# Kernel optimization log

Measured on AMD Instinct MI355X. Metric: run time of the kernel, lower is better.

Reference implementation:

```python
import jax, jax.numpy as jnp
import numpy as np

B, C, Wd, Hd = 128, 2048, 14, 14
S, L, M = 312, 300, 1024  # attributes, w2v length, med_dim
RATIO = 1.0               # attritube_num != 85 branch


def setup_inputs() -> dict:
    key = jax.random.key(0)
    ks = jax.random.split(key, 12)
    return {
        "feat": jax.random.normal(ks[0], (B, C, Wd, Hd), dtype=jnp.float32),
        "w2v_att": jax.random.normal(ks[1], (S, L), dtype=jnp.float32),
        "Wq": jax.random.normal(ks[2], (L, M), dtype=jnp.float32) * (1.0 / np.sqrt(L)),
        "bq": jax.random.normal(ks[3], (M,), dtype=jnp.float32) * 0.01,
        "Wk": jax.random.normal(ks[4], (C, M), dtype=jnp.float32) * (1.0 / np.sqrt(C)),
        "bk": jax.random.normal(ks[5], (M,), dtype=jnp.float32) * 0.01,
        "Wv": jax.random.normal(ks[6], (C, M), dtype=jnp.float32) * (1.0 / np.sqrt(C)),
        "bv": jax.random.normal(ks[7], (M,), dtype=jnp.float32) * 0.01,
        "Wo": jax.random.normal(ks[8], (M, C), dtype=jnp.float32) * (1.0 / np.sqrt(M)),
        "bo": jax.random.normal(ks[9], (C,), dtype=jnp.float32) * 0.01,
        "V_att_final": jax.random.normal(ks[10], (S, C), dtype=jnp.float32),
    }


def reference(feat, w2v_att, Wq, bq, Wk, bk, Wv, bv, Wo, bo, V_att_final):
    # feat: [B, C, W, H] -> [B, C, N]
    b, c = feat.shape[0], feat.shape[1]
    f = feat.reshape(b, c, -1)
    # Q from attribute word vectors: [S, M]
    query = w2v_att @ Wq + bq
    # K, V from spatial features: [B, N, M]
    key = jnp.einsum('bcn,cm->bnm', f, Wk) + bk
    value = jnp.einsum('bcn,cm->bnm', f, Wv) + bv
    # attention over spatial locations: [B, S, N]
    scores = jnp.einsum('sm,bnm->bsn', query, key)
    attention = jax.nn.softmax(scores, axis=-1)
    # attended features -> output projection: [B, S, C]
    attented = jnp.einsum('bsn,bnm->bsm', attention, value)
    attented_o = jnp.einsum('bsm,mc->bsc', attented, Wo) + bo
    # global average pool over spatial dims: [B, C]
    feat_pool = jnp.mean(f, axis=2)
    final = feat_pool[:, None, :] + RATIO * attented_o  # [B, S, C]
    # einsum classifier (hid_dim == 0 branch): [B, S]
    v2s = jnp.einsum('bsc,sc->bs', final, V_att_final)
    return v2s
```

## Files before the change

kernel.cpp:

```cpp
#include <hip/hip_runtime.h>
#include <hip/hip_bf16.h>

namespace {
constexpr int Bn = 128, Cn = 2048, Nn = 196, Sn = 312, Ln = 300, Mn = 1024;
constexpr int Sp = 320, Lp = 320, PR = 192;

constexpr size_t OFF_F16   = 0;
constexpr size_t OFF_POOLX = OFF_F16   + (size_t)Bn*Nn*Cn/2;
constexpr size_t OFF_HC    = OFF_POOLX + (size_t)PR*Cn/2;
constexpr size_t OFF_WVM   = OFF_HC    + (size_t)Cn*Lp/2;
constexpr size_t OFF_V16   = OFF_WVM   + (size_t)Sp*Mn/2;
constexpr size_t OFF_WV16  = OFF_V16   + (size_t)Sp*Cn/2;
constexpr size_t OFF_W2V   = OFF_WV16  + (size_t)Cn*Mn/2;
constexpr size_t OFF_BQK   = OFF_W2V   + (size_t)Sp*Lp/2;
constexpr size_t OFF_QK    = OFF_BQK   + Cn;
constexpr size_t OFF_WWT   = OFF_QK    + (size_t)Sp*Cn/2;
constexpr size_t OFF_PVF   = OFF_WWT   + (size_t)Sp*Cn/2;
}

typedef __attribute__((ext_vector_type(8))) short u16x8;
typedef __attribute__((ext_vector_type(8))) _Float16 f16x8;
typedef __attribute__((ext_vector_type(4))) _Float16 f16x4;
typedef __attribute__((ext_vector_type(4))) float f32x4;

__device__ __forceinline__ f16x8 as_h(u16x8 v) { return __builtin_bit_cast(f16x8, v); }

__device__ __forceinline__ void gload16(void* lds, const void* g) {
    __builtin_amdgcn_global_load_lds(
        (const __attribute__((address_space(1))) void*)g,
        (__attribute__((address_space(3))) void*)lds, 16, 0, 0);
}

__device__ __forceinline__ void stage_rows(ushort* lds, const ushort* src,
                                           size_t row0, int k0, int ld,
                                           int tid, int nslots) {
    int base = 0;
    for (; base + 256 <= nslots; base += 256) {
        const int slot = base + tid;
        const int r = slot >> 2, q = (slot & 3) ^ ((r >> 1) & 3);
        gload16(lds + (size_t)(base + (tid & 192)) * 8,
                src + (row0 + r) * (size_t)ld + k0 + q * 8);
    }
    const int rem = nslots - base;
    if (rem && tid < rem) {
        const int slot = base + tid;
        const int r = slot >> 2, q = (slot & 3) ^ ((r >> 1) & 3);
        gload16(lds + (size_t)base * 8,
                src + (row0 + r) * (size_t)ld + k0 + q * 8);
    }
}

__device__ __forceinline__ u16x8 frag_ld(const ushort* tile, int fr, int lane) {
    const int rl = lane & 15;
    const int q  = (lane >> 4) ^ ((rl >> 1) & 3);
    return *(const u16x8*)(tile + ((fr * 16 + rl) * 32 + q * 8));
}

__device__ __forceinline__ void mini16(
        const ushort* __restrict__ A, int lda, const ushort* __restrict__ B, int ldb,
        int r0, int c0, int K, const float* __restrict__ bias,
        _Float16* __restrict__ outh, float* __restrict__ outf, int ldo,
        ushort* sA, ushort* sB, int tid) {
    const int lane = tid & 63, wid = tid >> 6;
    f32x4 acc[2][2];
    #pragma unroll
    for (int i = 0; i < 2; ++i)
        #pragma unroll
        for (int j = 0; j < 2; ++j) acc[i][j] = (f32x4)0.f;
    const int fa = (wid >> 1) * 2, fb = (wid & 1) * 2;
    for (int k0 = 0; k0 < K; k0 += 32) {
        stage_rows(sA, A, r0, k0, lda, tid, 256);
        stage_rows(sB, B, c0, k0, ldb, tid, 256);
        __syncthreads();
        f16x8 a0 = as_h(frag_ld(sA, fa, lane)), a1 = as_h(frag_ld(sA, fa + 1, lane));
        f16x8 b0 = as_h(frag_ld(sB, fb, lane)), b1 = as_h(frag_ld(sB, fb + 1, lane));
        acc[0][0] = __builtin_amdgcn_mfma_f32_16x16x32_f16(a0, b0, acc[0][0], 0, 0, 0);
        acc[0][1] = __builtin_amdgcn_mfma_f32_16x16x32_f16(a0, b1, acc[0][1], 0, 0, 0);
        acc[1][0] = __builtin_amdgcn_mfma_f32_16x16x32_f16(a1, b0, acc[1][0], 0, 0, 0);
        acc[1][1] = __builtin_amdgcn_mfma_f32_16x16x32_f16(a1, b1, acc[1][1], 0, 0, 0);
        __syncthreads();
    }
    #pragma unroll
    for (int i = 0; i < 2; ++i)
        #pragma unroll
        for (int j = 0; j < 2; ++j)
            #pragma unroll
            for (int rr = 0; rr < 4; ++rr) {
                const size_t row = r0 + (wid >> 1) * 32 + i * 16 + (lane >> 4) * 4 + rr;
                const int col = c0 + (wid & 1) * 32 + j * 16 + (lane & 15);
                const float v = acc[i][j][rr] + (bias ? bias[col] : 0.f);
                if (outh) outh[row * ldo + col] = (_Float16)v;
                else      outf[row * ldo + col] = v;
            }
}

__device__ __forceinline__ void mini_f32in(
        const float* __restrict__ A, int lda, int RA,
        const float* __restrict__ B, int ldb, int RB,
        int r0, int c0, int K, _Float16* __restrict__ out, int ldo,
        ushort* sA, ushort* sB, int tid) {
    const int lane = tid & 63, wid = tid >> 6;
    f32x4 acc[2][2];
    #pragma unroll
    for (int i = 0; i < 2; ++i)
        #pragma unroll
        for (int j = 0; j < 2; ++j) acc[i][j] = (f32x4)0.f;
    const int fa = (wid >> 1) * 2, fb = (wid & 1) * 2;
    for (int k0 = 0; k0 < K; k0 += 32) {
        #pragma unroll
        for (int p = 0; p < 2; ++p) {
            const int e = tid + p * 256;
            const int r = e >> 3, k4 = (e & 7) * 4;
            const int ad = r * 32 + (((k4 >> 3) ^ ((r >> 1) & 3)) << 3) + (k4 & 7);
            float4 va = (r0 + r < RA) ? *(const float4*)&A[(size_t)(r0 + r) * lda + k0 + k4]
                                      : make_float4(0.f, 0.f, 0.f, 0.f);
            f16x4 ha;
            ha[0] = (_Float16)va.x; ha[1] = (_Float16)va.y;
            ha[2] = (_Float16)va.z; ha[3] = (_Float16)va.w;
            *(f16x4*)&sA[ad] = ha;
            float4 vb = (c0 + r < RB) ? *(const float4*)&B[(size_t)(c0 + r) * ldb + k0 + k4]
                                      : make_float4(0.f, 0.f, 0.f, 0.f);
            f16x4 hb;
            hb[0] = (_Float16)vb.x; hb[1] = (_Float16)vb.y;
            hb[2] = (_Float16)vb.z; hb[3] = (_Float16)vb.w;
            *(f16x4*)&sB[ad] = hb;
        }
        __syncthreads();
        f16x8 a0 = as_h(frag_ld(sA, fa, lane)), a1 = as_h(frag_ld(sA, fa + 1, lane));
        f16x8 b0 = as_h(frag_ld(sB, fb, lane)), b1 = as_h(frag_ld(sB, fb + 1, lane));
        acc[0][0] = __builtin_amdgcn_mfma_f32_16x16x32_f16(a0, b0, acc[0][0], 0, 0, 0);
        acc[0][1] = __builtin_amdgcn_mfma_f32_16x16x32_f16(a0, b1, acc[0][1], 0, 0, 0);
        acc[1][0] = __builtin_amdgcn_mfma_f32_16x16x32_f16(a1, b0, acc[1][0], 0, 0, 0);
        acc[1][1] = __builtin_amdgcn_mfma_f32_16x16x32_f16(a1, b1, acc[1][1], 0, 0, 0);
        __syncthreads();
    }
    #pragma unroll
    for (int i = 0; i < 2; ++i)
        #pragma unroll
        for (int j = 0; j < 2; ++j)
            #pragma unroll
            for (int rr = 0; rr < 4; ++rr) {
                const size_t row = r0 + (wid >> 1) * 32 + i * 16 + (lane >> 4) * 4 + rr;
                const int col = c0 + (wid & 1) * 32 + j * 16 + (lane & 15);
                out[row * ldo + col] = (_Float16)acc[i][j][rr];
            }
}

__global__ __launch_bounds__(256) void k_stageA(
        const float* __restrict__ feat, const float* __restrict__ w2v,
        const float* __restrict__ Wq,  const float* __restrict__ bq,
        const float* __restrict__ Wk,  const float* __restrict__ Wv,
        const float* __restrict__ bv,  const float* __restrict__ Wo,
        const float* __restrict__ bo,  const float* __restrict__ Vf,
        _Float16* __restrict__ f16, _Float16* __restrict__ poolx,
        _Float16* __restrict__ hc, _Float16* __restrict__ wvm,
        _Float16* __restrict__ v16, _Float16* __restrict__ wv16,
        _Float16* __restrict__ w2v16, float* __restrict__ bqk) {
    __shared__ __align__(16) char smem[51456];
    const int tid = threadIdx.x;
    int i = blockIdx.x;
    if (i < 8) {
        const int c = i * 256 + tid;
        float acc = bo[c];
        #pragma unroll 8
        for (int m = 0; m < Mn; ++m) acc = fmaf(bv[m], Wo[(size_t)m * Cn + c], acc);
        poolx[(size_t)128 * Cn + c] = (_Float16)acc;
    } else if ((i -= 8) < 512) {
        const int lane = tid & 63;
        const int c = i * 4 + (tid >> 6);
        float acc = 0.f;
        for (int m = lane; m < Mn; m += 64) acc = fmaf(bq[m], Wk[(size_t)c * Mn + m], acc);
        #pragma unroll
        for (int mm = 32; mm; mm >>= 1) acc += __shfl_xor(acc, mm);
        if (lane == 0) bqk[c] = acc;
    } else if ((i -= 512) < 160) {
        ushort* sA = (ushort*)smem;
        mini_f32in(Wk, Mn, 1 << 30, Wq, Mn, Ln,
                   (i / 5) * 64, (i % 5) * 64, Mn, hc, Lp, sA, sA + 2048, tid);
    } else if ((i -= 160) < 80) {
        ushort* sA = (ushort*)smem;
        mini_f32in(Vf, Cn, Sn, Wo, Cn, 1 << 30,
                   (i / 16) * 64, (i % 16) * 64, Cn, wvm, Mn, sA, sA + 2048, tid);
    } else if ((i -= 80) < 640) {
        const size_t idx = ((size_t)i * 256 + tid) * 4;
        const int r = (int)(idx >> 11);
        float4 v = (r < Sn) ? *(const float4*)&Vf[idx] : make_float4(0.f, 0.f, 0.f, 0.f);
        f16x4 h;
        h[0] = (_Float16)v.x; h[1] = (_Float16)v.y; h[2] = (_Float16)v.z; h[3] = (_Float16)v.w;
        *(f16x4*)&v16[idx] = h;
    } else if ((i -= 640) < 2048) {
        const size_t idx = ((size_t)i * 256 + tid) * 4;
        const float4 v = *(const float4*)&Wv[idx];
        f16x4 h;
        h[0] = (_Float16)v.x; h[1] = (_Float16)v.y; h[2] = (_Float16)v.z; h[3] = (_Float16)v.w;
        *(f16x4*)&wv16[idx] = h;
    } else if ((i -= 2048) < 100) {
        const int e0 = (i * 256 + tid) * 4;
        #pragma unroll
        for (int k = 0; k < 4; ++k) {
            const int e = e0 + k;
            const int r = e / Lp, cl = e - r * Lp;
            w2v16[e] = (r < Sn && cl < Ln) ? (_Float16)w2v[(size_t)r * Ln + cl] : (_Float16)0.f;
        }
    } else {
        i -= 100;
        float (*t)[197] = (float(*)[197])smem;
        float (*pp)[4]  = (float(*)[4])(smem + 64 * 197 * 4);
        const int b = i >> 5, c0 = (i & 31) * 64;
        for (int idx = tid; idx < 64 * 49; idx += 256) {
            const int r = idx / 49, nq = idx - r * 49;
            const float4 v = *(const float4*)&feat[((size_t)b * Cn + c0 + r) * Nn + nq * 4];
            t[r][nq * 4 + 0] = v.x; t[r][nq * 4 + 1] = v.y;
            t[r][nq * 4 + 2] = v.z; t[r][nq * 4 + 3] = v.w;
        }
        __syncthreads();
        {
            const int c = tid >> 2, q = tid & 3;
            float s = 0.f;
            #pragma unroll
            for (int n = 0; n < 49; ++n) s += t[c][q * 49 + n];
            pp[c][q] = s;
        }
        for (int idx = tid; idx < Nn * 32; idx += 256) {
            const int n = idx >> 5, cp = (idx & 31) * 2;
            f16x4 h;
            h[0] = (_Float16)t[cp][n]; h[1] = (_Float16)t[cp + 1][n];
            *(uint*)&f16[((size_t)b * Nn + n) * Cn + c0 + cp] = *(uint*)&h;
        }
        __syncthreads();
        if (tid < 64)
            poolx[(size_t)b * Cn + c0 + tid] =
                (_Float16)((pp[tid][0] + pp[tid][1] + pp[tid][2] + pp[tid][3]) * (1.0f / Nn));
    }
}

__global__ __launch_bounds__(256) void k_stageB(
        const ushort* __restrict__ w2v16, const ushort* __restrict__ hc,
        const float* __restrict__ bqk, const ushort* __restrict__ wvm,
        const ushort* __restrict__ wv16, const ushort* __restrict__ poolx,
        const ushort* __restrict__ v16,
        _Float16* __restrict__ qk16, _Float16* __restrict__ wwt16,
        float* __restrict__ pvf) {
    __shared__ __align__(16) ushort sA[2048], sB[2048];
    const int tid = threadIdx.x;
    int i = blockIdx.x;
    if (i < 160) {
        mini16(w2v16, Lp, hc, Lp, (i / 32) * 64, (i % 32) * 64, Lp,
               bqk, qk16, nullptr, Cn, sA, sB, tid);
    } else if ((i -= 160) < 160) {
        mini16(wvm, Mn, wv16, Mn, (i / 32) * 64, (i % 32) * 64, Mn,
               nullptr, wwt16, nullptr, Cn, sA, sB, tid);
    } else {
        i -= 160;
        mini16(poolx, Cn, v16, Cn, (i / 5) * 64, (i % 5) * 64, Cn,
               nullptr, nullptr, pvf, Sp, sA, sB, tid);
    }
}

__global__ __launch_bounds__(256) void k_attn(
        const _Float16* __restrict__ f16, const _Float16* __restrict__ qk16,
        const _Float16* __restrict__ ww16, const float* __restrict__ pvf,
        float* __restrict__ out) {
    __shared__ __align__(16) ushort smem[2][10752];
    const int tid = threadIdx.x, lane = tid & 63, wid = tid >> 6;
    const int id = blockIdx.x;
    const int xcd = id & 7, slot = id >> 3;
    const int b  = xcd * 16 + slot / 5;
    const int s0 = (slot % 5) * 64;
    const size_t frow0 = (size_t)b * Nn;

    f32x4 sc[13], vw[13];
    #pragma unroll
    for (int j = 0; j < 13; ++j) { sc[j] = (f32x4)0.f; vw[j] = (f32x4)0.f; }

    auto stage3 = [&](int p, int k0) {
        ushort* s = smem[p];
        stage_rows(s,        (const ushort*)f16,  frow0, k0, Cn, tid, 832);
        stage_rows(s + 6656, (const ushort*)qk16, s0,    k0, Cn, tid, 256);
        stage_rows(s + 8704, (const ushort*)ww16, s0,    k0, Cn, tid, 256);
    };

    constexpr int NIT = Cn / 32;
    stage3(0, 0);
    for (int t = 0; t < NIT; ++t) {
        const int cur = t & 1;
        __syncthreads();
        if (t + 1 < NIT) stage3(cur ^ 1, (t + 1) * 32);
        const ushort* sF = smem[cur];
        const f16x8 qf = as_h(frag_ld(sF + 6656, wid, lane));
        const f16x8 wf = as_h(frag_ld(sF + 8704, wid, lane));
        #pragma unroll
        for (int j = 0; j < 13; ++j) {
            const f16x8 ff = as_h(frag_ld(sF, j, lane));
            sc[j] = __builtin_amdgcn_mfma_f32_16x16x32_f16(qf, ff, sc[j], 0, 0, 0);
            vw[j] = __builtin_amdgcn_mfma_f32_16x16x32_f16(wf, ff, vw[j], 0, 0, 0);
        }
    }

    const int g = lane & 15;
    #pragma unroll
    for (int rr = 0; rr < 4; ++rr) {
        float mx = -1e30f;
        #pragma unroll
        for (int j = 0; j < 13; ++j)
            if (j < 12 || g < 4) mx = fmaxf(mx, sc[j][rr]);
        #pragma unroll
        for (int mm = 1; mm < 16; mm <<= 1) mx = fmaxf(mx, __shfl_xor(mx, mm));
        float den = 0.f, num = 0.f;
        #pragma unroll
        for (int j = 0; j < 13; ++j)
            if (j < 12 || g < 4) {
                const float e = __expf(sc[j][rr] - mx);
                den += e;
                num = fmaf(e, vw[j][rr], num);
            }
        #pragma unroll
        for (int mm = 1; mm < 16; mm <<= 1) {
            den += __shfl_xor(den, mm);
            num += __shfl_xor(num, mm);
        }
        if (g == 0) {
            const int s = s0 + wid * 16 + (lane >> 4) * 4 + rr;
            if (s < Sn)
                out[(size_t)b * Sn + s] =
                    pvf[(size_t)b * Sp + s] + pvf[(size_t)128 * Sp + s] + num / den;
        }
    }
}

extern "C" void kernel_launch(void* const* d_in, const int* in_sizes, int n_in,
                              void* d_out, int out_size, void* d_ws, size_t ws_size,
                              hipStream_t stream) {
    (void)in_sizes; (void)n_in; (void)ws_size; (void)out_size;
    const float* feat = (const float*)d_in[0];
    const float* w2v  = (const float*)d_in[1];
    const float* Wq   = (const float*)d_in[2];
    const float* bq   = (const float*)d_in[3];
    const float* Wk   = (const float*)d_in[4];
    const float* Wv   = (const float*)d_in[6];
    const float* bv   = (const float*)d_in[7];
    const float* Wo   = (const float*)d_in[8];
    const float* bo   = (const float*)d_in[9];
    const float* Vf   = (const float*)d_in[10];
    float* out = (float*)d_out;
    float* ws  = (float*)d_ws;

    _Float16* f16   = (_Float16*)(ws + OFF_F16);
    _Float16* poolx = (_Float16*)(ws + OFF_POOLX);
    _Float16* hc    = (_Float16*)(ws + OFF_HC);
    _Float16* wvm   = (_Float16*)(ws + OFF_WVM);
    _Float16* v16   = (_Float16*)(ws + OFF_V16);
    _Float16* wv16  = (_Float16*)(ws + OFF_WV16);
    _Float16* w2v16 = (_Float16*)(ws + OFF_W2V);
    float*    bqk   = ws + OFF_BQK;
    _Float16* qk16  = (_Float16*)(ws + OFF_QK);
    _Float16* wwt16 = (_Float16*)(ws + OFF_WWT);
    float*    pvf   = ws + OFF_PVF;

    k_stageA<<<dim3(8 + 512 + 160 + 80 + 640 + 2048 + 100 + 4096), 256, 0, stream>>>(
        feat, w2v, Wq, bq, Wk, Wv, bv, Wo, bo, Vf,
        f16, poolx, hc, wvm, v16, wv16, w2v16, bqk);
    k_stageB<<<dim3(160 + 160 + 15), 256, 0, stream>>>(
        (const ushort*)w2v16, (const ushort*)hc, bqk, (const ushort*)wvm,
        (const ushort*)wv16, (const ushort*)poolx, (const ushort*)v16,
        qk16, wwt16, pvf);
    k_attn<<<dim3(640), 256, 0, stream>>>(f16, qk16, wwt16, pvf, out);
}
```

Before: 247.8 us.

## Fuse fp16 feature conversion and pooled term into attention kernel

Drops the separate pass that transposed and converted feat to an fp16 [B,N,C] buffer and computed pooled features. The attention kernel now reads fp32 feat directly, converts and transposes it into LDS through a register-staged double buffer, and computes the pooled·V term with an extra MFMA over the same feature tiles. The bias constant (bo·V plus bv·Wo·V) is computed per attribute in a small reduction. This removes a large intermediate write and read of the features, at the cost of more register pressure, larger LDS use and extra conversion work inside the main loop.

Result: slower. 271.7 us (+9.6%).

```diff
diff --git a/kernel.cpp b/kernel.cpp
--- a/kernel.cpp
+++ b/kernel.cpp
@@ -3,24 +3,23 @@
 
 namespace {
 constexpr int Bn = 128, Cn = 2048, Nn = 196, Sn = 312, Ln = 300, Mn = 1024;
-constexpr int Sp = 320, Lp = 320, PR = 192;
-
-constexpr size_t OFF_F16   = 0;
-constexpr size_t OFF_POOLX = OFF_F16   + (size_t)Bn*Nn*Cn/2;
-constexpr size_t OFF_HC    = OFF_POOLX + (size_t)PR*Cn/2;
-constexpr size_t OFF_WVM   = OFF_HC    + (size_t)Cn*Lp/2;
-constexpr size_t OFF_V16   = OFF_WVM   + (size_t)Sp*Mn/2;
-constexpr size_t OFF_WV16  = OFF_V16   + (size_t)Sp*Cn/2;
-constexpr size_t OFF_W2V   = OFF_WV16  + (size_t)Cn*Mn/2;
-constexpr size_t OFF_BQK   = OFF_W2V   + (size_t)Sp*Lp/2;
-constexpr size_t OFF_QK    = OFF_BQK   + Cn;
-constexpr size_t OFF_WWT   = OFF_QK    + (size_t)Sp*Cn/2;
-constexpr size_t OFF_PVF   = OFF_WWT   + (size_t)Sp*Cn/2;
+constexpr int Sp = 320, Lp = 320;
+
+constexpr size_t OFF_HC   = 0;
+constexpr size_t OFF_WVM  = OFF_HC  + (size_t)Cn*Lp/2;
+constexpr size_t OFF_V16  = OFF_WVM + (size_t)Sp*Mn/2;
+constexpr size_t OFF_WV16 = OFF_V16 + (size_t)Sp*Cn/2;
+constexpr size_t OFF_W2V  = OFF_WV16+ (size_t)Cn*Mn/2;
+constexpr size_t OFF_BQK  = OFF_W2V + (size_t)Sp*Lp/2;
+constexpr size_t OFF_QK   = OFF_BQK + Cn;
+constexpr size_t OFF_WWT  = OFF_QK  + (size_t)Sp*Cn/2;
+constexpr size_t OFF_CST  = OFF_WWT + (size_t)Sp*Cn/2;
 }
 
 typedef __attribute__((ext_vector_type(8))) short u16x8;
 typedef __attribute__((ext_vector_type(8))) _Float16 f16x8;
 typedef __attribute__((ext_vector_type(4))) _Float16 f16x4;
+typedef __attribute__((ext_vector_type(2))) _Float16 f16x2;
 typedef __attribute__((ext_vector_type(4))) float f32x4;
 
 __device__ __forceinline__ f16x8 as_h(u16x8 v) { return __builtin_bit_cast(f16x8, v); }
@@ -147,25 +146,23 @@
 }
 
 __global__ __launch_bounds__(256) void k_stageA(
-        const float* __restrict__ feat, const float* __restrict__ w2v,
-        const float* __restrict__ Wq,  const float* __restrict__ bq,
-        const float* __restrict__ Wk,  const float* __restrict__ Wv,
-        const float* __restrict__ bv,  const float* __restrict__ Wo,
-        const float* __restrict__ bo,  const float* __restrict__ Vf,
-        _Float16* __restrict__ f16, _Float16* __restrict__ poolx,
+        const float* __restrict__ w2v, const float* __restrict__ Wq,
+        const float* __restrict__ bq,  const float* __restrict__ Wk,
+        const float* __restrict__ Wv,  const float* __restrict__ Wo,
+        const float* __restrict__ Vf,
         _Float16* __restrict__ hc, _Float16* __restrict__ wvm,
         _Float16* __restrict__ v16, _Float16* __restrict__ wv16,
         _Float16* __restrict__ w2v16, float* __restrict__ bqk) {
-    __shared__ __align__(16) char smem[51456];
+    __shared__ __align__(16) ushort sm[4096];
     const int tid = threadIdx.x;
     int i = blockIdx.x;
-    if (i < 8) {
-        const int c = i * 256 + tid;
-        float acc = bo[c];
-        #pragma unroll 8
-        for (int m = 0; m < Mn; ++m) acc = fmaf(bv[m], Wo[(size_t)m * Cn + c], acc);
-        poolx[(size_t)128 * Cn + c] = (_Float16)acc;
-    } else if ((i -= 8) < 512) {
+    if (i < 160) {
+        mini_f32in(Wk, Mn, 1 << 30, Wq, Mn, Ln,
+                   (i / 5) * 64, (i % 5) * 64, Mn, hc, Lp, sm, sm + 2048, tid);
+    } else if ((i -= 160) < 80) {
+        mini_f32in(Vf, Cn, Sn, Wo, Cn, 1 << 30,
+                   (i / 16) * 64, (i % 16) * 64, Cn, wvm, Mn, sm, sm + 2048, tid);
+    } else if ((i -= 80) < 512) {
         const int lane = tid & 63;
         const int c = i * 4 + (tid >> 6);
         float acc = 0.f;
@@ -173,15 +170,7 @@
         #pragma unroll
         for (int mm = 32; mm; mm >>= 1) acc += __shfl_xor(acc, mm);
         if (lane == 0) bqk[c] = acc;
-    } else if ((i -= 512) < 160) {
-        ushort* sA = (ushort*)smem;
-        mini_f32in(Wk, Mn, 1 << 30, Wq, Mn, Ln,
-                   (i / 5) * 64, (i % 5) * 64, Mn, hc, Lp, sA, sA + 2048, tid);
-    } else if ((i -= 160) < 80) {
-        ushort* sA = (ushort*)smem;
-        mini_f32in(Vf, Cn, Sn, Wo, Cn, 1 << 30,
-                   (i / 16) * 64, (i % 16) * 64, Cn, wvm, Mn, sA, sA + 2048, tid);
-    } else if ((i -= 80) < 640) {
+    } else if ((i -= 512) < 640) {
         const size_t idx = ((size_t)i * 256 + tid) * 4;
         const int r = (int)(idx >> 11);
         float4 v = (r < Sn) ? *(const float4*)&Vf[idx] : make_float4(0.f, 0.f, 0.f, 0.f);
@@ -194,7 +183,8 @@
         f16x4 h;
         h[0] = (_Float16)v.x; h[1] = (_Float16)v.y; h[2] = (_Float16)v.z; h[3] = (_Float16)v.w;
         *(f16x4*)&wv16[idx] = h;
-    } else if ((i -= 2048) < 100) {
+    } else {
+        i -= 2048;
         const int e0 = (i * 256 + tid) * 4;
         #pragma unroll
         for (int k = 0; k < 4; ++k) {
@@ -202,99 +192,124 @@
             const int r = e / Lp, cl = e - r * Lp;
             w2v16[e] = (r < Sn && cl < Ln) ? (_Float16)w2v[(size_t)r * Ln + cl] : (_Float16)0.f;
         }
-    } else {
-        i -= 100;
-        float (*t)[197] = (float(*)[197])smem;
-        float (*pp)[4]  = (float(*)[4])(smem + 64 * 197 * 4);
-        const int b = i >> 5, c0 = (i & 31) * 64;
-        for (int idx = tid; idx < 64 * 49; idx += 256) {
-            const int r = idx / 49, nq = idx - r * 49;
-            const float4 v = *(const float4*)&feat[((size_t)b * Cn + c0 + r) * Nn + nq * 4];
-            t[r][nq * 4 + 0] = v.x; t[r][nq * 4 + 1] = v.y;
-            t[r][nq * 4 + 2] = v.z; t[r][nq * 4 + 3] = v.w;
-        }
-        __syncthreads();
-        {
-            const int c = tid >> 2, q = tid & 3;
-            float s = 0.f;
-            #pragma unroll
-            for (int n = 0; n < 49; ++n) s += t[c][q * 49 + n];
-            pp[c][q] = s;
-        }
-        for (int idx = tid; idx < Nn * 32; idx += 256) {
-            const int n = idx >> 5, cp = (idx & 31) * 2;
-            f16x4 h;
-            h[0] = (_Float16)t[cp][n]; h[1] = (_Float16)t[cp + 1][n];
-            *(uint*)&f16[((size_t)b * Nn + n) * Cn + c0 + cp] = *(uint*)&h;
-        }
-        __syncthreads();
-        if (tid < 64)
-            poolx[(size_t)b * Cn + c0 + tid] =
-                (_Float16)((pp[tid][0] + pp[tid][1] + pp[tid][2] + pp[tid][3]) * (1.0f / Nn));
     }
 }
 
 __global__ __launch_bounds__(256) void k_stageB(
         const ushort* __restrict__ w2v16, const ushort* __restrict__ hc,
         const float* __restrict__ bqk, const ushort* __restrict__ wvm,
-        const ushort* __restrict__ wv16, const ushort* __restrict__ poolx,
-        const ushort* __restrict__ v16,
+        const ushort* __restrict__ wv16,
+        const float* __restrict__ bo, const float* __restrict__ Vf,
+        const float* __restrict__ bv,
         _Float16* __restrict__ qk16, _Float16* __restrict__ wwt16,
-        float* __restrict__ pvf) {
+        float* __restrict__ cst) {
     __shared__ __align__(16) ushort sA[2048], sB[2048];
     const int tid = threadIdx.x;
     int i = blockIdx.x;
     if (i < 160) {
+        mini16(wvm, Mn, wv16, Mn, (i / 32) * 64, (i % 32) * 64, Mn,
+               nullptr, wwt16, nullptr, Cn, sA, sB, tid);
+    } else if ((i -= 160) < 160) {
         mini16(w2v16, Lp, hc, Lp, (i / 32) * 64, (i % 32) * 64, Lp,
                bqk, qk16, nullptr, Cn, sA, sB, tid);
-    } else if ((i -= 160) < 160) {
-        mini16(wvm, Mn, wv16, Mn, (i / 32) * 64, (i % 32) * 64, Mn,
-               nullptr, wwt16, nullptr, Cn, sA, sB, tid);
     } else {
         i -= 160;
-        mini16(poolx, Cn, v16, Cn, (i / 5) * 64, (i % 5) * 64, Cn,
-               nullptr, nullptr, pvf, Sp, sA, sB, tid);
+        const int lane = tid & 63, wid = tid >> 6;
+        const int s = i * 4 + wid;
+        if (s >= Sn) return;
+        float part = 0.f;
+        for (int c = lane; c < Cn; c += 64) part = fmaf(bo[c], Vf[(size_t)s * Cn + c], part);
+        for (int m = lane; m < Mn; m += 64)
+            part = fmaf(bv[m], (float)*(const _Float16*)&wvm[(size_t)s * Mn + m], part);
+        #pragma unroll
+        for (int mm = 32; mm; mm >>= 1) part += __shfl_xor(part, mm);
+        if (lane == 0) cst[s] = part;
     }
 }
 
 __global__ __launch_bounds__(256) void k_attn(
-        const _Float16* __restrict__ f16, const _Float16* __restrict__ qk16,
-        const _Float16* __restrict__ ww16, const float* __restrict__ pvf,
-        float* __restrict__ out) {
-    __shared__ __align__(16) ushort smem[2][10752];
+        const float* __restrict__ feat, const _Float16* __restrict__ qk16,
+        const _Float16* __restrict__ ww16, const _Float16* __restrict__ v16,
+        const float* __restrict__ cst, float* __restrict__ out) {
+    __shared__ __align__(16) ushort smem[2][12800];
     const int tid = threadIdx.x, lane = tid & 63, wid = tid >> 6;
     const int id = blockIdx.x;
     const int xcd = id & 7, slot = id >> 3;
     const int b  = xcd * 16 + slot / 5;
     const int s0 = (slot % 5) * 64;
-    const size_t frow0 = (size_t)b * Nn;
-
-    f32x4 sc[13], vw[13];
+    const float* featb = feat + (size_t)b * Cn * Nn;
+
+    for (int u = tid; u < 384; u += 256) {
+        const int bf = u / 192, w = u - bf * 192;
+        *(uint*)&smem[bf][196 * 32 + w * 2] = 0u;
+    }
+
+    f32x4 sc[13], vw[13], gv = (f32x4)0.f;
     #pragma unroll
     for (int j = 0; j < 13; ++j) { sc[j] = (f32x4)0.f; vw[j] = (f32x4)0.f; }
 
-    auto stage3 = [&](int p, int k0) {
-        ushort* s = smem[p];
-        stage_rows(s,        (const ushort*)f16,  frow0, k0, Cn, tid, 832);
-        stage_rows(s + 6656, (const ushort*)qk16, s0,    k0, Cn, tid, 256);
-        stage_rows(s + 8704, (const ushort*)ww16, s0,    k0, Cn, tid, 256);
+    const int p = tid & 15, grp = tid >> 4;
+    float4 lo[4], hi[4];
+
+    auto loadF = [&](int k0) {
+        #pragma unroll
+        for (int it = 0; it < 4; ++it) {
+            const int qp = grp + 16 * it;
+            if (qp < 49) {
+                lo[it] = *(const float4*)&featb[(size_t)(k0 + 2 * p) * Nn + qp * 4];
+                hi[it] = *(const float4*)&featb[(size_t)(k0 + 2 * p + 1) * Nn + qp * 4];
+            }
+        }
     };
+    auto writeF = [&](int pb) {
+        ushort* s = smem[pb];
+        #pragma unroll
+        for (int it = 0; it < 4; ++it) {
+            const int qp = grp + 16 * it;
+            if (qp < 49) {
+                const float* fl = (const float*)&lo[it];
+                const float* fh = (const float*)&hi[it];
+                #pragma unroll
+                for (int k = 0; k < 4; ++k) {
+                    const int r = qp * 4 + k;
+                    const int qs = (p >> 2) ^ ((r >> 1) & 3);
+                    f16x2 h; h[0] = (_Float16)fl[k]; h[1] = (_Float16)fh[k];
+                    *(uint*)&s[r * 32 + qs * 8 + 2 * (p & 3)] = __builtin_bit_cast(uint, h);
+                }
+            }
+        }
+    };
+    auto stageQWV = [&](int pb, int k0) {
+        ushort* s = smem[pb];
+        stage_rows(s + 6656,  (const ushort*)qk16, s0, k0, Cn, tid, 256);
+        stage_rows(s + 8704,  (const ushort*)ww16, s0, k0, Cn, tid, 256);
+        stage_rows(s + 10752, (const ushort*)v16,  s0, k0, Cn, tid, 256);
+    };
+
+    loadF(0);
+    writeF(0);
+    stageQWV(0, 0);
 
     constexpr int NIT = Cn / 32;
-    stage3(0, 0);
     for (int t = 0; t < NIT; ++t) {
         const int cur = t & 1;
         __syncthreads();
-        if (t + 1 < NIT) stage3(cur ^ 1, (t + 1) * 32);
+        if (t + 1 < NIT) {
+            loadF((t + 1) * 32);
+            stageQWV(cur ^ 1, (t + 1) * 32);
+        }
         const ushort* sF = smem[cur];
-        const f16x8 qf = as_h(frag_ld(sF + 6656, wid, lane));
-        const f16x8 wf = as_h(frag_ld(sF + 8704, wid, lane));
+        const f16x8 qf = as_h(frag_ld(sF + 6656,  wid, lane));
+        const f16x8 wf = as_h(frag_ld(sF + 8704,  wid, lane));
+        const f16x8 vf = as_h(frag_ld(sF + 10752, wid, lane));
         #pragma unroll
         for (int j = 0; j < 13; ++j) {
             const f16x8 ff = as_h(frag_ld(sF, j, lane));
             sc[j] = __builtin_amdgcn_mfma_f32_16x16x32_f16(qf, ff, sc[j], 0, 0, 0);
             vw[j] = __builtin_amdgcn_mfma_f32_16x16x32_f16(wf, ff, vw[j], 0, 0, 0);
-        }
+            gv    = __builtin_amdgcn_mfma_f32_16x16x32_f16(vf, ff, gv,    0, 0, 0);
+        }
+        if (t + 1 < NIT) writeF(cur ^ 1);
     }
 
     const int g = lane & 15;
@@ -314,16 +329,17 @@
                 den += e;
                 num = fmaf(e, vw[j][rr], num);
             }
+        float gs = gv[rr];
         #pragma unroll
         for (int mm = 1; mm < 16; mm <<= 1) {
             den += __shfl_xor(den, mm);
             num += __shfl_xor(num, mm);
+            gs  += __shfl_xor(gs, mm);
         }
         if (g == 0) {
             const int s = s0 + wid * 16 + (lane >> 4) * 4 + rr;
             if (s < Sn)
-                out[(size_t)b * Sn + s] =
-                    pvf[(size_t)b * Sp + s] + pvf[(size_t)128 * Sp + s] + num / den;
+                out[(size_t)b * Sn + s] = cst[s] + gs * (1.0f / Nn) + num / den;
         }
     }
 }
@@ -345,8 +361,6 @@
     float* out = (float*)d_out;
     float* ws  = (float*)d_ws;
 
-    _Float16* f16   = (_Float16*)(ws + OFF_F16);
-    _Float16* poolx = (_Float16*)(ws + OFF_POOLX);
     _Float16* hc    = (_Float16*)(ws + OFF_HC);
     _Float16* wvm   = (_Float16*)(ws + OFF_WVM);
     _Float16* v16   = (_Float16*)(ws + OFF_V16);
@@ -355,14 +369,12 @@
     float*    bqk   = ws + OFF_BQK;
     _Float16* qk16  = (_Float16*)(ws + OFF_QK);
     _Float16* wwt16 = (_Float16*)(ws + OFF_WWT);
-    float*    pvf   = ws + OFF_PVF;
-
-    k_stageA<<<dim3(8 + 512 + 160 + 80 + 640 + 2048 + 100 + 4096), 256, 0, stream>>>(
-        feat, w2v, Wq, bq, Wk, Wv, bv, Wo, bo, Vf,
-        f16, poolx, hc, wvm, v16, wv16, w2v16, bqk);
-    k_stageB<<<dim3(160 + 160 + 15), 256, 0, stream>>>(
+    float*    cst   = ws + OFF_CST;
+
+    k_stageA<<<dim3(160 + 80 + 512 + 640 + 2048 + 100), 256, 0, stream>>>(
+        w2v, Wq, bq, Wk, Wv, Wo, Vf, hc, wvm, v16, wv16, w2v16, bqk);
+    k_stageB<<<dim3(160 + 160 + 78), 256, 0, stream>>>(
         (const ushort*)w2v16, (const ushort*)hc, bqk, (const ushort*)wvm,
-        (const ushort*)wv16, (const ushort*)poolx, (const ushort*)v16,
-        qk16, wwt16, pvf);
-    k_attn<<<dim3(640), 256, 0, stream>>>(f16, qk16, wwt16, pvf, out);
-}
+        (const ushort*)wv16, bo, Vf, bv, qk16, wwt16, cst);
+    k_attn<<<dim3(640), 256, 0, stream>>>(feat, qk16, wwt16, v16, cst, out);
+}
```

## Tile f16 feature layout into 64-channel blocks and double-buffer stage GEMMs

Applied to the files above, without the earlier changes.

The transposed fp16 feature buffer is stored as contiguous 196x64 channel blocks per batch, so k_attn loads each K-slice from a compact region instead of striding across full 2048-channel rows. The mini16 GEMM gains LDS double buffering with one barrier per iteration, and mini_f32in prefetches the next fp32 tile into registers before the MFMAs. Stage-B blocks are reordered so the long K=2048 pooled-feature GEMM launches first. This adds LDS and register pressure, and the new addressing must stay consistent between the producer and consumer of the feature buffer.

Result: faster. 216.6 us (median of 2 runs) (-12.6%).

```diff
diff --git a/kernel.cpp b/kernel.cpp
--- a/kernel.cpp
+++ b/kernel.cpp
@@ -60,7 +60,7 @@
         const ushort* __restrict__ A, int lda, const ushort* __restrict__ B, int ldb,
         int r0, int c0, int K, const float* __restrict__ bias,
         _Float16* __restrict__ outh, float* __restrict__ outf, int ldo,
-        ushort* sA, ushort* sB, int tid) {
+        ushort* sm, int tid) {
     const int lane = tid & 63, wid = tid >> 6;
     f32x4 acc[2][2];
     #pragma unroll
@@ -68,17 +68,24 @@
         #pragma unroll
         for (int j = 0; j < 2; ++j) acc[i][j] = (f32x4)0.f;
     const int fa = (wid >> 1) * 2, fb = (wid & 1) * 2;
-    for (int k0 = 0; k0 < K; k0 += 32) {
-        stage_rows(sA, A, r0, k0, lda, tid, 256);
-        stage_rows(sB, B, c0, k0, ldb, tid, 256);
-        __syncthreads();
+    const int NI = K / 32;
+    stage_rows(sm,        A, r0, 0, lda, tid, 256);
+    stage_rows(sm + 2048, B, c0, 0, ldb, tid, 256);
+    for (int t = 0; t < NI; ++t) {
+        const int cur = (t & 1) * 4096;
+        __syncthreads();
+        if (t + 1 < NI) {
+            stage_rows(sm + (cur ^ 4096),        A, r0, (t + 1) * 32, lda, tid, 256);
+            stage_rows(sm + (cur ^ 4096) + 2048, B, c0, (t + 1) * 32, ldb, tid, 256);
+        }
+        const ushort* sA = sm + cur;
+        const ushort* sB = sm + cur + 2048;
         f16x8 a0 = as_h(frag_ld(sA, fa, lane)), a1 = as_h(frag_ld(sA, fa + 1, lane));
         f16x8 b0 = as_h(frag_ld(sB, fb, lane)), b1 = as_h(frag_ld(sB, fb + 1, lane));
         acc[0][0] = __builtin_amdgcn_mfma_f32_16x16x32_f16(a0, b0, acc[0][0], 0, 0, 0);
         acc[0][1] = __builtin_amdgcn_mfma_f32_16x16x32_f16(a0, b1, acc[0][1], 0, 0, 0);
         acc[1][0] = __builtin_amdgcn_mfma_f32_16x16x32_f16(a1, b0, acc[1][0], 0, 0, 0);
         acc[1][1] = __builtin_amdgcn_mfma_f32_16x16x32_f16(a1, b1, acc[1][1], 0, 0, 0);
-        __syncthreads();
     }
     #pragma unroll
     for (int i = 0; i < 2; ++i)
@@ -106,26 +113,37 @@
         #pragma unroll
         for (int j = 0; j < 2; ++j) acc[i][j] = (f32x4)0.f;
     const int fa = (wid >> 1) * 2, fb = (wid & 1) * 2;
+
+    float4 va[2], vb[2];
+    auto loadregs = [&](int k0) {
+        #pragma unroll
+        for (int p = 0; p < 2; ++p) {
+            const int e = tid + p * 256;
+            const int r = e >> 3, k4 = (e & 7) * 4;
+            va[p] = (r0 + r < RA) ? *(const float4*)&A[(size_t)(r0 + r) * lda + k0 + k4]
+                                  : make_float4(0.f, 0.f, 0.f, 0.f);
+            vb[p] = (c0 + r < RB) ? *(const float4*)&B[(size_t)(c0 + r) * ldb + k0 + k4]
+                                  : make_float4(0.f, 0.f, 0.f, 0.f);
+        }
+    };
+    loadregs(0);
     for (int k0 = 0; k0 < K; k0 += 32) {
         #pragma unroll
         for (int p = 0; p < 2; ++p) {
             const int e = tid + p * 256;
             const int r = e >> 3, k4 = (e & 7) * 4;
             const int ad = r * 32 + (((k4 >> 3) ^ ((r >> 1) & 3)) << 3) + (k4 & 7);
-            float4 va = (r0 + r < RA) ? *(const float4*)&A[(size_t)(r0 + r) * lda + k0 + k4]
-                                      : make_float4(0.f, 0.f, 0.f, 0.f);
             f16x4 ha;
-            ha[0] = (_Float16)va.x; ha[1] = (_Float16)va.y;
-            ha[2] = (_Float16)va.z; ha[3] = (_Float16)va.w;
+            ha[0] = (_Float16)va[p].x; ha[1] = (_Float16)va[p].y;
+            ha[2] = (_Float16)va[p].z; ha[3] = (_Float16)va[p].w;
             *(f16x4*)&sA[ad] = ha;
-            float4 vb = (c0 + r < RB) ? *(const float4*)&B[(size_t)(c0 + r) * ldb + k0 + k4]
-                                      : make_float4(0.f, 0.f, 0.f, 0.f);
             f16x4 hb;
-            hb[0] = (_Float16)vb.x; hb[1] = (_Float16)vb.y;
-            hb[2] = (_Float16)vb.z; hb[3] = (_Float16)vb.w;
+            hb[0] = (_Float16)vb[p].x; hb[1] = (_Float16)vb[p].y;
+            hb[2] = (_Float16)vb[p].z; hb[3] = (_Float16)vb[p].w;
             *(f16x4*)&sB[ad] = hb;
         }
         __syncthreads();
+        if (k0 + 32 < K) loadregs(k0 + 32);
         f16x8 a0 = as_h(frag_ld(sA, fa, lane)), a1 = as_h(frag_ld(sA, fa + 1, lane));
         f16x8 b0 = as_h(frag_ld(sB, fb, lane)), b1 = as_h(frag_ld(sB, fb + 1, lane));
         acc[0][0] = __builtin_amdgcn_mfma_f32_16x16x32_f16(a0, b0, acc[0][0], 0, 0, 0);
@@ -221,11 +239,12 @@
             for (int n = 0; n < 49; ++n) s += t[c][q * 49 + n];
             pp[c][q] = s;
         }
+        ushort* outb = (ushort*)f16 + ((size_t)(b * 32) + (c0 >> 6)) * (196 * 64);
         for (int idx = tid; idx < Nn * 32; idx += 256) {
             const int n = idx >> 5, cp = (idx & 31) * 2;
             f16x4 h;
             h[0] = (_Float16)t[cp][n]; h[1] = (_Float16)t[cp + 1][n];
-            *(uint*)&f16[((size_t)b * Nn + n) * Cn + c0 + cp] = *(uint*)&h;
+            *(uint*)&outb[(size_t)n * 64 + cp] = *(uint*)&h;
         }
         __syncthreads();
         if (tid < 64)
@@ -241,19 +260,19 @@
         const ushort* __restrict__ v16,
         _Float16* __restrict__ qk16, _Float16* __restrict__ wwt16,
         float* __restrict__ pvf) {
-    __shared__ __align__(16) ushort sA[2048], sB[2048];
+    __shared__ __align__(16) ushort sm[8192];
     const int tid = threadIdx.x;
     int i = blockIdx.x;
-    if (i < 160) {
-        mini16(w2v16, Lp, hc, Lp, (i / 32) * 64, (i % 32) * 64, Lp,
-               bqk, qk16, nullptr, Cn, sA, sB, tid);
-    } else if ((i -= 160) < 160) {
+    if (i < 15) {
+        mini16(poolx, Cn, v16, Cn, (i / 5) * 64, (i % 5) * 64, Cn,
+               nullptr, nullptr, pvf, Sp, sm, tid);
+    } else if ((i -= 15) < 160) {
         mini16(wvm, Mn, wv16, Mn, (i / 32) * 64, (i % 32) * 64, Mn,
-               nullptr, wwt16, nullptr, Cn, sA, sB, tid);
+               nullptr, wwt16, nullptr, Cn, sm, tid);
     } else {
         i -= 160;
-        mini16(poolx, Cn, v16, Cn, (i / 5) * 64, (i % 5) * 64, Cn,
-               nullptr, nullptr, pvf, Sp, sA, sB, tid);
+        mini16(w2v16, Lp, hc, Lp, (i / 32) * 64, (i % 32) * 64, Lp,
+               bqk, qk16, nullptr, Cn, sm, tid);
     }
 }
 
@@ -264,10 +283,9 @@
     __shared__ __align__(16) ushort smem[2][10752];
     const int tid = threadIdx.x, lane = tid & 63, wid = tid >> 6;
     const int id = blockIdx.x;
-    const int xcd = id & 7, slot = id >> 3;
-    const int b  = xcd * 16 + slot / 5;
-    const int s0 = (slot % 5) * 64;
-    const size_t frow0 = (size_t)b * Nn;
+    const int xcd = id & 7, slot0 = id >> 3;
+    const int b  = xcd * 16 + slot0 / 5;
+    const int s0 = (slot0 % 5) * 64;
 
     f32x4 sc[13], vw[13];
     #pragma unroll
@@ -275,9 +293,23 @@
 
     auto stage3 = [&](int p, int k0) {
         ushort* s = smem[p];
-        stage_rows(s,        (const ushort*)f16,  frow0, k0, Cn, tid, 832);
-        stage_rows(s + 6656, (const ushort*)qk16, s0,    k0, Cn, tid, 256);
-        stage_rows(s + 8704, (const ushort*)ww16, s0,    k0, Cn, tid, 256);
+        const ushort* fbase = (const ushort*)f16 +
+            ((size_t)(b * 32) + (k0 >> 6)) * (196 * 64) + ((k0 >> 5) & 1) * 32;
+        int base = 0;
+        for (; base + 256 <= 832; base += 256) {
+            const int sl = base + tid;
+            const int r = sl >> 2, q = (sl & 3) ^ ((r >> 1) & 3);
+            const int rc = r < 196 ? r : 195;
+            gload16(s + (size_t)(base + (tid & 192)) * 8, fbase + rc * 64 + q * 8);
+        }
+        if (tid < 64) {
+            const int sl = base + tid;
+            const int r = sl >> 2, q = (sl & 3) ^ ((r >> 1) & 3);
+            const int rc = r < 196 ? r : 195;
+            gload16(s + (size_t)base * 8, fbase + rc * 64 + q * 8);
+        }
+        stage_rows(s + 6656, (const ushort*)qk16, s0, k0, Cn, tid, 256);
+        stage_rows(s + 8704, (const ushort*)ww16, s0, k0, Cn, tid, 256);
     };
 
     constexpr int NIT = Cn / 32;
@@ -360,7 +392,7 @@
     k_stageA<<<dim3(8 + 512 + 160 + 80 + 640 + 2048 + 100 + 4096), 256, 0, stream>>>(
         feat, w2v, Wq, bq, Wk, Wv, bv, Wo, bo, Vf,
         f16, poolx, hc, wvm, v16, wv16, w2v16, bqk);
-    k_stageB<<<dim3(160 + 160 + 15), 256, 0, stream>>>(
+    k_stageB<<<dim3(15 + 160 + 160), 256, 0, stream>>>(
         (const ushort*)w2v16, (const ushort*)hc, bqk, (const ushort*)wvm,
         (const ushort*)wv16, (const ushort*)poolx, (const ushort*)v16,
         qk16, wwt16, pvf);
```
